# Kernel tuning notes

Hardware: AMD Instinct MI355X
Metric: run time of the kernel (lower is better)

Reference implementation:

```python
import jax, jax.numpy as jnp
import numpy as np

N_NODES = 50000
N_EDGES = 500000
D_IN = 128
HID = 128
OUT = 2
N_REL = 4
BN_EPS = 1e-5


def setup_inputs() -> dict:
    key = jax.random.key(0)
    ks = jax.random.split(key, 14)
    s_in = 1.0 / np.sqrt(D_IN)
    s_h = 1.0 / np.sqrt(HID)
    return {
        "x": jax.random.normal(ks[0], (N_NODES, D_IN), jnp.float32),
        "edge_index": jax.random.randint(ks[1], (N_REL, 2, N_EDGES), 0, N_NODES, jnp.int32),
        "W1": jax.random.normal(ks[2], (N_REL, D_IN, HID), jnp.float32) * s_in,
        "b1": jax.random.normal(ks[3], (N_REL, HID), jnp.float32) * s_in,
        "W2": jax.random.normal(ks[4], (N_REL, HID, HID), jnp.float32) * s_h,
        "b2": jax.random.normal(ks[5], (N_REL, HID), jnp.float32) * s_h,
        "bn_gamma": jnp.ones((HID,), jnp.float32),
        "bn_beta": jnp.zeros((HID,), jnp.float32),
        "lin1_W": jax.random.normal(ks[6], (HID, HID), jnp.float32) * s_h,
        "lin1_b": jax.random.normal(ks[7], (HID,), jnp.float32) * s_h,
        "lin2_W": jax.random.normal(ks[8], (HID, OUT), jnp.float32) * s_h,
        "lin2_b": jax.random.normal(ks[9], (OUT,), jnp.float32) * s_h,
    }


def _gcn(x, ei, W, b):
    # GCNConv: D^-1/2 (A + I) D^-1/2 (X W) + b
    n = x.shape[0]
    h = x @ W                                    # [N, H]
    loops = jnp.arange(n, dtype=ei.dtype)
    src = jnp.concatenate([ei[0], loops])        # add self loops
    dst = jnp.concatenate([ei[1], loops])
    deg = jax.ops.segment_sum(jnp.ones(dst.shape, h.dtype), dst, num_segments=n)
    dinv = jnp.where(deg > 0, jax.lax.rsqrt(deg), 0.0)
    norm = dinv[src] * dinv[dst]                 # [E+N]
    msg = h[src] * norm[:, None]                 # gather + scale
    return jax.ops.segment_sum(msg, dst, num_segments=n) + b


def _hetero(x, edge_index, W, b):
    # HeteroConv with aggr='sum' over the 4 relation types (same src/dst node type)
    out = _gcn(x, edge_index[0], W[0], b[0])
    for r in range(1, N_REL):
        out = out + _gcn(x, edge_index[r], W[r], b[r])
    return out


def reference(x, edge_index, W1, b1, W2, b2, bn_gamma, bn_beta, lin1_W, lin1_b, lin2_W, lin2_b):
    h = jax.nn.relu(_hetero(x, edge_index, W1, b1))
    h = jax.nn.relu(_hetero(h, edge_index, W2, b2))
    # BatchNorm1d (batch statistics, biased variance)
    mean = h.mean(axis=0)
    var = h.var(axis=0)
    h = (h - mean) * jax.lax.rsqrt(var + BN_EPS) * bn_gamma + bn_beta
    h = jax.nn.relu(h @ lin1_W + lin1_b)
    # dropout is identity in eval
    return h @ lin2_W + lin2_b
```

## Files before the change

kernel.cpp:

```cpp
#include <hip/hip_runtime.h>
#include <math.h>

#define NN 50000
#define NE 500000
#define NREL 4
#define D 128
#define RSZ 512
#define NRANGE 98
#define NBK (NREL * NRANGE)
#define BCAP 6144
#define NCH 128
#define CH 3907
#define FCAP 96
#define CAST_BLKS 6250
static constexpr float BN_EPS = 1e-5f;

typedef __attribute__((ext_vector_type(8))) _Float16 half8;
typedef __attribute__((ext_vector_type(4))) float f32x4;

__device__ __forceinline__ unsigned short f2h_bits(float f) {
    _Float16 h = (_Float16)f;
    return __builtin_bit_cast(unsigned short, h);
}

__global__ __launch_bounds__(256) void k_pre(const float* __restrict__ x,
                                             const float* __restrict__ W1, const float* __restrict__ W2,
                                             const float* __restrict__ l1W, const float* __restrict__ b1,
                                             const float* __restrict__ b2,
                                             unsigned short* __restrict__ xb,
                                             unsigned short* __restrict__ Wt1,
                                             unsigned short* __restrict__ Wt2,
                                             unsigned short* __restrict__ Wt3,
                                             float* __restrict__ bs1, float* __restrict__ bs2,
                                             float* __restrict__ bnsum) {
    int blk = blockIdx.x, tid = threadIdx.x;
    if (blk < CAST_BLKS) {
        int i = blk * 256 + tid;
        float4 v = *(const float4*)(x + (size_t)i * 4);
        unsigned short u[4] = {f2h_bits(v.x), f2h_bits(v.y), f2h_bits(v.z), f2h_bits(v.w)};
        *(ushort4*)(xb + (size_t)i * 4) = *(ushort4*)u;
    } else if (blk < CAST_BLKS + 256) {
        int i = (blk - CAST_BLKS) * 256 + tid;
        int kk = i & 511, n = i >> 9;
        Wt1[n * 512 + kk] = f2h_bits(W1[kk * 128 + n]);
        Wt2[n * 512 + kk] = f2h_bits(W2[kk * 128 + n]);
    } else if (blk < CAST_BLKS + 320) {
        int i = (blk - CAST_BLKS - 256) * 256 + tid;
        int kk = i & 127, n = i >> 7;
        Wt3[n * 128 + kk] = f2h_bits(l1W[kk * 128 + n]);
    } else {
        if (tid < 128) {
            bs1[tid] = b1[tid] + b1[128 + tid] + b1[256 + tid] + b1[384 + tid];
            bs2[tid] = b2[tid] + b2[128 + tid] + b2[256 + tid] + b2[384 + tid];
        }
        bnsum[tid] = 0.f;
    }
}

__global__ __launch_bounds__(256) void k_bin(const int* __restrict__ ei,
                                             int* __restrict__ frag,
                                             int* __restrict__ cntg) {
    int c = blockIdx.x, r = blockIdx.y;
    const int* srcp = ei + r * 2 * NE;
    const int* dstp = srcp + NE;
    __shared__ int bins[NRANGE * FCAP];
    __shared__ int cnt[NRANGE];
    int tid = threadIdx.x;
    for (int i = tid; i < NRANGE; i += 256) cnt[i] = 0;
    __syncthreads();
    int e0 = c * CH, e1 = min(e0 + CH, NE);
    for (int e = e0 + tid; e < e1; e += 256) {
        int d = dstp[e];
        int s = srcp[e];
        int q = d >> 9;
        int pos = atomicAdd(&cnt[q], 1);
        if (pos < FCAP) bins[q * FCAP + pos] = s | ((d & 511) << 16);
    }
    __syncthreads();
    int w = tid >> 6, lane = tid & 63;
    for (int q = w; q < NRANGE; q += 4) {
        int k = min(cnt[q], FCAP);
        int gbase = ((r * NRANGE + q) * NCH + c) * FCAP;
        for (int i = lane; i < k; i += 64) frag[gbase + i] = bins[q * FCAP + i];
    }
    for (int q = tid; q < NRANGE; q += 256) cntg[(r * NRANGE + q) * NCH + c] = min(cnt[q], FCAP);
}

__global__ __launch_bounds__(512) void k_sortb(const int* __restrict__ frag,
                                               const int* __restrict__ cntg,
                                               unsigned short* __restrict__ csr,
                                               int* __restrict__ rstart,
                                               int* __restrict__ rend,
                                               float* __restrict__ dinv) {
    int q = blockIdx.x, r = blockIdx.y;
    int blk = r * NRANGE + q;
    int n0 = q * RSZ;
    int nrows = min(RSZ, NN - n0);
    __shared__ int cnts[NCH], cbase[NCH];
    __shared__ int stage[BCAP];
    __shared__ unsigned short csr_s[BCAP];
    __shared__ int hist[RSZ], off[RSZ], cnt2[RSZ];
    int tid = threadIdx.x;
    hist[tid] = 0;
    cnt2[tid] = 0;
    if (tid < NCH) cnts[tid] = cntg[blk * NCH + tid];
    __syncthreads();
    if (tid < NCH) cbase[tid] = cnts[tid];
    __syncthreads();
    for (int d = 1; d < NCH; d <<= 1) {
        int t = 0;
        if (tid < NCH && tid >= d) t = cbase[tid - d];
        __syncthreads();
        if (tid < NCH) cbase[tid] += t;
        __syncthreads();
    }
    if (tid < NCH) cbase[tid] -= cnts[tid];
    __syncthreads();
    int tot = cbase[NCH - 1] + cnts[NCH - 1];
    {
        int g = tid >> 2, l = tid & 3;
        int k = cnts[g], cb = cbase[g];
        int gbase = (blk * NCH + g) * FCAP;
        for (int i = l; i < k; i += 4)
            if (cb + i < BCAP) stage[cb + i] = frag[gbase + i];
    }
    __syncthreads();
    if (tot > BCAP) tot = BCAP;
    for (int i = tid; i < tot; i += 512) atomicAdd(&hist[(stage[i] >> 16) & 511], 1);
    __syncthreads();
    int h = hist[tid];
    if (tid < nrows) dinv[r * NN + n0 + tid] = rsqrtf((float)(h + 1));
    off[tid] = h;
    __syncthreads();
    for (int d = 1; d < RSZ; d <<= 1) {
        int t = (tid >= d) ? off[tid - d] : 0;
        __syncthreads();
        off[tid] += t;
        __syncthreads();
    }
    int excl = off[tid] - h;
    __syncthreads();
    off[tid] = excl;
    int base = blk * BCAP;
    if (tid < nrows) {
        rstart[r * NN + n0 + tid] = base + excl;
        rend[r * NN + n0 + tid] = base + excl + h;
    }
    __syncthreads();
    for (int i = tid; i < tot; i += 512) {
        int v = stage[i];
        int dl = (v >> 16) & 511;
        int p = atomicAdd(&cnt2[dl], 1);
        csr_s[off[dl] + p] = (unsigned short)(v & 0xFFFF);
    }
    __syncthreads();
    for (int i = tid; i < tot; i += 512) csr[base + i] = csr_s[i];
}

__global__ __launch_bounds__(256) void k_wei(const unsigned short* __restrict__ csr,
                                             const float* __restrict__ dinv,
                                             float* __restrict__ wcsr) {
    int gi = blockIdx.x * 256 + threadIdx.x;
    int r = gi / (NRANGE * BCAP);
    int s = csr[gi];
    wcsr[gi] = dinv[r * NN + min(s, NN - 1)];
}

__global__ __launch_bounds__(256) void k_agg(const unsigned short* __restrict__ in,
                                             const unsigned short* __restrict__ csr,
                                             const float* __restrict__ wcsr,
                                             const int* __restrict__ rstart,
                                             const int* __restrict__ rend,
                                             const float* __restrict__ dinv,
                                             unsigned short* __restrict__ Acat) {
    int r = blockIdx.y;
    int wave = threadIdx.x >> 6, lane = threadIdx.x & 63;
    int n = blockIdx.x * 4 + wave;
    if (n >= NN) return;
    int nb = r * NN + n;
    int q = lane >> 4, t = lane & 15;
    const half8* in8 = (const half8*)in;
    half8 us = in8[(size_t)n * 16 + t];
    float wn = dinv[nb];
    int start = rstart[nb], end = rend[nb];
    int deg = end - start;
    float a[8];
#pragma unroll
    for (int j = 0; j < 8; j++) a[j] = 0.f;
    for (int w0 = 0; w0 < deg; w0 += 64) {
        int li = w0 + lane;
        int sv = 0;
        float wv = 0.f;
        if (li < deg) {
            sv = csr[start + li];
            wv = wcsr[start + li];
        }
        int cnt = min(deg - w0, 64);
        for (int b = 0; b < cnt; b += 16) {
            int e = b + q * 4;
            int s0 = __shfl(sv, e + 0), s1 = __shfl(sv, e + 1);
            int s2 = __shfl(sv, e + 2), s3 = __shfl(sv, e + 3);
            float f0 = __shfl(wv, e + 0), f1 = __shfl(wv, e + 1);
            float f2 = __shfl(wv, e + 2), f3 = __shfl(wv, e + 3);
            half8 u0 = in8[s0 * 16 + t];
            half8 u1 = in8[s1 * 16 + t];
            half8 u2 = in8[s2 * 16 + t];
            half8 u3 = in8[s3 * 16 + t];
#pragma unroll
            for (int j = 0; j < 8; j++) a[j] = fmaf((float)u0[j], f0, a[j]);
#pragma unroll
            for (int j = 0; j < 8; j++) a[j] = fmaf((float)u1[j], f1, a[j]);
#pragma unroll
            for (int j = 0; j < 8; j++) a[j] = fmaf((float)u2[j], f2, a[j]);
#pragma unroll
            for (int j = 0; j < 8; j++) a[j] = fmaf((float)u3[j], f3, a[j]);
        }
    }
#pragma unroll
    for (int j = 0; j < 8; j++) {
        a[j] += __shfl_xor(a[j], 16);
        a[j] += __shfl_xor(a[j], 32);
    }
    if (q == 0) {
        _Float16 ob[8];
#pragma unroll
        for (int j = 0; j < 8; j++)
            ob[j] = (_Float16)(wn * fmaf((float)us[j], wn, a[j]));
        *(half8*)(Acat + (size_t)n * 512 + r * 128 + t * 8) = *(half8*)ob;
    }
}

template <int K, bool STATS>
__global__ __launch_bounds__(256) void k_mm(const unsigned short* __restrict__ A,
                                            const unsigned short* __restrict__ Bt,
                                            const float* __restrict__ bias,
                                            unsigned short* __restrict__ C,
                                            float* __restrict__ bnsum) {
    int tid = threadIdx.x;
    int w = tid >> 6, lane = tid & 63;
    int ln = lane & 15, quad = lane >> 4;
    int mwave = blockIdx.x * 256 + w * 64;

    f32x4 acc[4][8];
#pragma unroll
    for (int a = 0; a < 4; a++)
#pragma unroll
        for (int b = 0; b < 8; b++) acc[a][b] = (f32x4){0.f, 0.f, 0.f, 0.f};

    size_t arow[4];
#pragma unroll
    for (int mf = 0; mf < 4; mf++) {
        int m = mwave + mf * 16 + ln;
        arow[mf] = (size_t)min(m, NN - 1) * K;
    }
    size_t brow[8];
#pragma unroll
    for (int nf = 0; nf < 8; nf++) brow[nf] = (size_t)(nf * 16 + ln) * K;

    for (int k0 = 0; k0 < K; k0 += 32) {
        int kof = k0 + quad * 8;
        half8 af[4], bf[8];
#pragma unroll
        for (int mf = 0; mf < 4; mf++) af[mf] = *(const half8*)(A + arow[mf] + kof);
#pragma unroll
        for (int nf = 0; nf < 8; nf++) bf[nf] = *(const half8*)(Bt + brow[nf] + kof);
#pragma unroll
        for (int mf = 0; mf < 4; mf++)
#pragma unroll
            for (int nf = 0; nf < 8; nf++)
                acc[mf][nf] = __builtin_amdgcn_mfma_f32_16x16x32_f16(af[mf], bf[nf], acc[mf][nf], 0, 0, 0);
    }

    float bs[8];
#pragma unroll
    for (int nf = 0; nf < 8; nf++) bs[nf] = bias[nf * 16 + ln];
    float sn[8], qn[8];
#pragma unroll
    for (int nf = 0; nf < 8; nf++) { sn[nf] = 0.f; qn[nf] = 0.f; }

#pragma unroll
    for (int mf = 0; mf < 4; mf++)
#pragma unroll
        for (int nf = 0; nf < 8; nf++)
#pragma unroll
            for (int rg = 0; rg < 4; rg++) {
                int m = mwave + mf * 16 + quad * 4 + rg;
                if (m < NN) {
                    float v = fmaxf(acc[mf][nf][rg] + bs[nf], 0.f);
                    if (STATS) { sn[nf] += v; qn[nf] += v * v; }
                    C[(size_t)m * 128 + nf * 16 + ln] = f2h_bits(v);
                }
            }

    if (STATS) {
#pragma unroll
        for (int nf = 0; nf < 8; nf++) {
            float s = sn[nf], q = qn[nf];
            s += __shfl_xor(s, 16); s += __shfl_xor(s, 32);
            q += __shfl_xor(q, 16); q += __shfl_xor(q, 32);
            if (quad == 0) {
                unsafeAtomicAdd(&bnsum[nf * 16 + ln], s);
                unsafeAtomicAdd(&bnsum[128 + nf * 16 + ln], q);
            }
        }
    }
}

__global__ __launch_bounds__(256) void k_final(const unsigned short* __restrict__ R2,
                                               const float* __restrict__ bnsum,
                                               const float* __restrict__ gamma,
                                               const float* __restrict__ beta,
                                               const unsigned short* __restrict__ Wt3,
                                               const float* __restrict__ l1b,
                                               const float* __restrict__ l2W,
                                               const float* __restrict__ l2b,
                                               float* __restrict__ out) {
    __shared__ float bnp_s[256];
    int tid = threadIdx.x;
    if (tid < 128) {
        float mean = bnsum[tid] / (float)NN;
        float var = bnsum[128 + tid] / (float)NN - mean * mean;
        float sc = gamma[tid] * rsqrtf(var + BN_EPS);
        bnp_s[tid] = sc;
        bnp_s[128 + tid] = beta[tid] - mean * sc;
    }
    __syncthreads();
    int w = tid >> 6, lane = tid & 63;
    int ln = lane & 15, quad = lane >> 4;
    int mwave = blockIdx.x * 256 + w * 64;

    f32x4 acc[4][8];
#pragma unroll
    for (int a = 0; a < 4; a++)
#pragma unroll
        for (int b = 0; b < 8; b++) acc[a][b] = (f32x4){0.f, 0.f, 0.f, 0.f};

    size_t arow[4];
#pragma unroll
    for (int mf = 0; mf < 4; mf++) {
        int m = mwave + mf * 16 + ln;
        arow[mf] = (size_t)min(m, NN - 1) * 128;
    }
    size_t brow[8];
#pragma unroll
    for (int nf = 0; nf < 8; nf++) brow[nf] = (size_t)(nf * 16 + ln) * 128;

    for (int k0 = 0; k0 < 128; k0 += 32) {
        int kof = k0 + quad * 8;
        float scv[8], shv[8];
#pragma unroll
        for (int j = 0; j < 8; j++) {
            scv[j] = bnp_s[kof + j];
            shv[j] = bnp_s[128 + kof + j];
        }
        half8 af[4], bf[8];
#pragma unroll
        for (int mf = 0; mf < 4; mf++) {
            half8 rv = *(const half8*)(R2 + arow[mf] + kof);
            _Float16 ab[8];
#pragma unroll
            for (int j = 0; j < 8; j++)
                ab[j] = (_Float16)(fmaf((float)rv[j], scv[j], shv[j]));
            af[mf] = *(half8*)ab;
        }
#pragma unroll
        for (int nf = 0; nf < 8; nf++) bf[nf] = *(const half8*)(Wt3 + brow[nf] + kof);
#pragma unroll
        for (int mf = 0; mf < 4; mf++)
#pragma unroll
            for (int nf = 0; nf < 8; nf++)
                acc[mf][nf] = __builtin_amdgcn_mfma_f32_16x16x32_f16(af[mf], bf[nf], acc[mf][nf], 0, 0, 0);
    }

    float b1v[8], w0[8], w1[8];
#pragma unroll
    for (int nf = 0; nf < 8; nf++) {
        int n = nf * 16 + ln;
        b1v[nf] = l1b[n];
        w0[nf] = l2W[n * 2];
        w1[nf] = l2W[n * 2 + 1];
    }
    float ob0 = l2b[0], ob1 = l2b[1];
#pragma unroll
    for (int mf = 0; mf < 4; mf++)
#pragma unroll
        for (int rg = 0; rg < 4; rg++) {
            float p0 = 0.f, p1 = 0.f;
#pragma unroll
            for (int nf = 0; nf < 8; nf++) {
                float y = fmaxf(acc[mf][nf][rg] + b1v[nf], 0.f);
                p0 += y * w0[nf];
                p1 += y * w1[nf];
            }
            p0 += __shfl_xor(p0, 1); p0 += __shfl_xor(p0, 2);
            p0 += __shfl_xor(p0, 4); p0 += __shfl_xor(p0, 8);
            p1 += __shfl_xor(p1, 1); p1 += __shfl_xor(p1, 2);
            p1 += __shfl_xor(p1, 4); p1 += __shfl_xor(p1, 8);
            int m = mwave + mf * 16 + quad * 4 + rg;
            if (ln == 0 && m < NN) {
                out[(size_t)m * 2 + 0] = p0 + ob0;
                out[(size_t)m * 2 + 1] = p1 + ob1;
            }
        }
}

extern "C" void kernel_launch(void* const* d_in, const int* in_sizes, int n_in,
                              void* d_out, int out_size, void* d_ws, size_t ws_size,
                              hipStream_t stream) {
    const float* x = (const float*)d_in[0];
    const int* ei = (const int*)d_in[1];
    const float* W1 = (const float*)d_in[2];
    const float* b1 = (const float*)d_in[3];
    const float* W2 = (const float*)d_in[4];
    const float* b2 = (const float*)d_in[5];
    const float* gamma = (const float*)d_in[6];
    const float* beta = (const float*)d_in[7];
    const float* l1W = (const float*)d_in[8];
    const float* l1b = (const float*)d_in[9];
    const float* l2W = (const float*)d_in[10];
    const float* l2b = (const float*)d_in[11];
    float* out = (float*)d_out;

    char* ws = (char*)d_ws;
    size_t off = 0;
    auto alloc = [&](size_t bytes) {
        void* p = ws + off;
        off += (bytes + 255) & ~(size_t)255;
        return p;
    };
    float* dinv = (float*)alloc((size_t)NREL * NN * sizeof(float));
    int* rstart = (int*)alloc((size_t)NREL * NN * sizeof(int));
    int* rend = (int*)alloc((size_t)NREL * NN * sizeof(int));
    unsigned short* csr = (unsigned short*)alloc((size_t)NBK * BCAP * 2);
    unsigned short* xb = (unsigned short*)alloc((size_t)NN * D * 2);
    unsigned short* Acat = (unsigned short*)alloc((size_t)NN * 512 * 2);
    unsigned short* h1b = (unsigned short*)alloc((size_t)NN * D * 2);
    unsigned short* R2b = (unsigned short*)alloc((size_t)NN * D * 2);
    unsigned short* Wt1 = (unsigned short*)alloc(128 * 512 * 2);
    unsigned short* Wt2 = (unsigned short*)alloc(128 * 512 * 2);
    unsigned short* Wt3 = (unsigned short*)alloc(128 * 128 * 2);
    float* bs1 = (float*)alloc(128 * sizeof(float));
    float* bs2 = (float*)alloc(128 * sizeof(float));
    float* bnsum = (float*)alloc(256 * sizeof(float));

    int* frag = (int*)Acat;
    int* cntg = frag + (size_t)NREL * NRANGE * NCH * FCAP;
    float* wcsr = (float*)R2b;

    k_pre<<<CAST_BLKS + 321, 256, 0, stream>>>(x, W1, W2, l1W, b1, b2, xb, Wt1, Wt2, Wt3,
                                               bs1, bs2, bnsum);
    dim3 bgrid(NCH, NREL);
    k_bin<<<bgrid, 256, 0, stream>>>(ei, frag, cntg);
    dim3 sgrid(NRANGE, NREL);
    k_sortb<<<sgrid, 512, 0, stream>>>(frag, cntg, csr, rstart, rend, dinv);
    k_wei<<<(NBK * BCAP) / 256, 256, 0, stream>>>(csr, dinv, wcsr);

    dim3 agrid((NN + 3) / 4, NREL);
    k_agg<<<agrid, 256, 0, stream>>>(xb, csr, wcsr, rstart, rend, dinv, Acat);
    k_mm<512, false><<<(NN + 255) / 256, 256, 0, stream>>>(Acat, Wt1, bs1, h1b, nullptr);
    k_agg<<<agrid, 256, 0, stream>>>(h1b, csr, wcsr, rstart, rend, dinv, Acat);
    k_mm<512, true><<<(NN + 255) / 256, 256, 0, stream>>>(Acat, Wt2, bs2, R2b, bnsum);
    k_final<<<(NN + 255) / 256, 256, 0, stream>>>(R2b, bnsum, gamma, beta, Wt3, l1b, l2W, l2b, out);
}
```

Baseline: 387.0 us.

## Pack CSR index and fp16 weight; aggregate all relations per node in one wave

k_wei now writes a single 32-bit word per edge, holding the 16-bit source index and an fp16 normalization weight, in place of separate index and float-weight arrays. k_agg drops the relation grid dimension: each 16-lane quarter of a wave handles one relation for the same node, and the loop runs to the maximum degree across the four relations. Each step processes 8 or 16 gathers per quarter, and the self-loop term is folded into the accumulator initialization. This removes the cross-quarter reduction, halves the edge metadata loads, and gives more gathers in flight per lane. In exchange, quarters with lower degree sit idle while the wave covers the longest relation, and the edge weight is stored in reduced fp16 precision.

```diff
diff --git a/kernel.cpp b/kernel.cpp
--- a/kernel.cpp
+++ b/kernel.cpp
@@ -21,6 +21,9 @@
 __device__ __forceinline__ unsigned short f2h_bits(float f) {
     _Float16 h = (_Float16)f;
     return __builtin_bit_cast(unsigned short, h);
+}
+__device__ __forceinline__ float hi2f(unsigned p) {
+    return (float)__builtin_bit_cast(_Float16, (unsigned short)(p >> 16));
 }
 
 __global__ __launch_bounds__(256) void k_pre(const float* __restrict__ x,
@@ -159,75 +162,113 @@
 
 __global__ __launch_bounds__(256) void k_wei(const unsigned short* __restrict__ csr,
                                              const float* __restrict__ dinv,
-                                             float* __restrict__ wcsr) {
+                                             unsigned* __restrict__ wpack) {
     int gi = blockIdx.x * 256 + threadIdx.x;
     int r = gi / (NRANGE * BCAP);
     int s = csr[gi];
-    wcsr[gi] = dinv[r * NN + min(s, NN - 1)];
+    float w = dinv[r * NN + min(s, NN - 1)];
+    wpack[gi] = (unsigned)s | ((unsigned)f2h_bits(w) << 16);
 }
 
 __global__ __launch_bounds__(256) void k_agg(const unsigned short* __restrict__ in,
-                                             const unsigned short* __restrict__ csr,
-                                             const float* __restrict__ wcsr,
+                                             const unsigned* __restrict__ wpack,
                                              const int* __restrict__ rstart,
                                              const int* __restrict__ rend,
                                              const float* __restrict__ dinv,
                                              unsigned short* __restrict__ Acat) {
-    int r = blockIdx.y;
     int wave = threadIdx.x >> 6, lane = threadIdx.x & 63;
     int n = blockIdx.x * 4 + wave;
     if (n >= NN) return;
-    int nb = r * NN + n;
-    int q = lane >> 4, t = lane & 15;
+    int t = lane & 15;
+    int base = lane & 48;
+    int nb = (base >> 4) * NN + n;
     const half8* in8 = (const half8*)in;
+    float wn = dinv[nb];
+    int start = rstart[nb];
+    int deg = rend[nb] - start;
+    int dm = deg;
+    dm = max(dm, __shfl_xor(dm, 16));
+    dm = max(dm, __shfl_xor(dm, 32));
     half8 us = in8[(size_t)n * 16 + t];
-    float wn = dinv[nb];
-    int start = rstart[nb], end = rend[nb];
-    int deg = end - start;
     float a[8];
 #pragma unroll
-    for (int j = 0; j < 8; j++) a[j] = 0.f;
-    for (int w0 = 0; w0 < deg; w0 += 64) {
-        int li = w0 + lane;
-        int sv = 0;
-        float wv = 0.f;
-        if (li < deg) {
-            sv = csr[start + li];
-            wv = wcsr[start + li];
-        }
-        int cnt = min(deg - w0, 64);
-        for (int b = 0; b < cnt; b += 16) {
-            int e = b + q * 4;
-            int s0 = __shfl(sv, e + 0), s1 = __shfl(sv, e + 1);
-            int s2 = __shfl(sv, e + 2), s3 = __shfl(sv, e + 3);
-            float f0 = __shfl(wv, e + 0), f1 = __shfl(wv, e + 1);
-            float f2 = __shfl(wv, e + 2), f3 = __shfl(wv, e + 3);
-            half8 u0 = in8[s0 * 16 + t];
-            half8 u1 = in8[s1 * 16 + t];
-            half8 u2 = in8[s2 * 16 + t];
-            half8 u3 = in8[s3 * 16 + t];
-#pragma unroll
-            for (int j = 0; j < 8; j++) a[j] = fmaf((float)u0[j], f0, a[j]);
-#pragma unroll
-            for (int j = 0; j < 8; j++) a[j] = fmaf((float)u1[j], f1, a[j]);
-#pragma unroll
-            for (int j = 0; j < 8; j++) a[j] = fmaf((float)u2[j], f2, a[j]);
-#pragma unroll
-            for (int j = 0; j < 8; j++) a[j] = fmaf((float)u3[j], f3, a[j]);
-        }
-    }
-#pragma unroll
-    for (int j = 0; j < 8; j++) {
-        a[j] += __shfl_xor(a[j], 16);
-        a[j] += __shfl_xor(a[j], 32);
-    }
-    if (q == 0) {
-        _Float16 ob[8];
-#pragma unroll
-        for (int j = 0; j < 8; j++)
-            ob[j] = (_Float16)(wn * fmaf((float)us[j], wn, a[j]));
-        *(half8*)(Acat + (size_t)n * 512 + r * 128 + t * 8) = *(half8*)ob;
-    }
+    for (int j = 0; j < 8; j++) a[j] = wn * (float)us[j];
+
+    for (int w0 = 0; w0 < dm; w0 += 16) {
+        int li = w0 + t;
+        int gi = min(start + li, NBK * BCAP - 1);
+        unsigned pv = wpack[gi];
+        if (li >= deg) pv = 0u;
+        unsigned p0 = __shfl(pv, base + 0), p1 = __shfl(pv, base + 1);
+        unsigned p2 = __shfl(pv, base + 2), p3 = __shfl(pv, base + 3);
+        unsigned p4 = __shfl(pv, base + 4), p5 = __shfl(pv, base + 5);
+        unsigned p6 = __shfl(pv, base + 6), p7 = __shfl(pv, base + 7);
+        {
+            half8 r0 = in8[(p0 & 0xFFFFu) * 16 + t];
+            half8 r1 = in8[(p1 & 0xFFFFu) * 16 + t];
+            half8 r2 = in8[(p2 & 0xFFFFu) * 16 + t];
+            half8 r3 = in8[(p3 & 0xFFFFu) * 16 + t];
+            half8 r4 = in8[(p4 & 0xFFFFu) * 16 + t];
+            half8 r5 = in8[(p5 & 0xFFFFu) * 16 + t];
+            half8 r6 = in8[(p6 & 0xFFFFu) * 16 + t];
+            half8 r7 = in8[(p7 & 0xFFFFu) * 16 + t];
+            float w0f = hi2f(p0), w1f = hi2f(p1), w2f = hi2f(p2), w3f = hi2f(p3);
+            float w4f = hi2f(p4), w5f = hi2f(p5), w6f = hi2f(p6), w7f = hi2f(p7);
+#pragma unroll
+            for (int j = 0; j < 8; j++) a[j] = fmaf((float)r0[j], w0f, a[j]);
+#pragma unroll
+            for (int j = 0; j < 8; j++) a[j] = fmaf((float)r1[j], w1f, a[j]);
+#pragma unroll
+            for (int j = 0; j < 8; j++) a[j] = fmaf((float)r2[j], w2f, a[j]);
+#pragma unroll
+            for (int j = 0; j < 8; j++) a[j] = fmaf((float)r3[j], w3f, a[j]);
+#pragma unroll
+            for (int j = 0; j < 8; j++) a[j] = fmaf((float)r4[j], w4f, a[j]);
+#pragma unroll
+            for (int j = 0; j < 8; j++) a[j] = fmaf((float)r5[j], w5f, a[j]);
+#pragma unroll
+            for (int j = 0; j < 8; j++) a[j] = fmaf((float)r6[j], w6f, a[j]);
+#pragma unroll
+            for (int j = 0; j < 8; j++) a[j] = fmaf((float)r7[j], w7f, a[j]);
+        }
+        if (w0 + 8 >= dm) continue;
+        p0 = __shfl(pv, base + 8);  p1 = __shfl(pv, base + 9);
+        p2 = __shfl(pv, base + 10); p3 = __shfl(pv, base + 11);
+        p4 = __shfl(pv, base + 12); p5 = __shfl(pv, base + 13);
+        p6 = __shfl(pv, base + 14); p7 = __shfl(pv, base + 15);
+        {
+            half8 r0 = in8[(p0 & 0xFFFFu) * 16 + t];
+            half8 r1 = in8[(p1 & 0xFFFFu) * 16 + t];
+            half8 r2 = in8[(p2 & 0xFFFFu) * 16 + t];
+            half8 r3 = in8[(p3 & 0xFFFFu) * 16 + t];
+            half8 r4 = in8[(p4 & 0xFFFFu) * 16 + t];
+            half8 r5 = in8[(p5 & 0xFFFFu) * 16 + t];
+            half8 r6 = in8[(p6 & 0xFFFFu) * 16 + t];
+            half8 r7 = in8[(p7 & 0xFFFFu) * 16 + t];
+            float w0f = hi2f(p0), w1f = hi2f(p1), w2f = hi2f(p2), w3f = hi2f(p3);
+            float w4f = hi2f(p4), w5f = hi2f(p5), w6f = hi2f(p6), w7f = hi2f(p7);
+#pragma unroll
+            for (int j = 0; j < 8; j++) a[j] = fmaf((float)r0[j], w0f, a[j]);
+#pragma unroll
+            for (int j = 0; j < 8; j++) a[j] = fmaf((float)r1[j], w1f, a[j]);
+#pragma unroll
+            for (int j = 0; j < 8; j++) a[j] = fmaf((float)r2[j], w2f, a[j]);
+#pragma unroll
+            for (int j = 0; j < 8; j++) a[j] = fmaf((float)r3[j], w3f, a[j]);
+#pragma unroll
+            for (int j = 0; j < 8; j++) a[j] = fmaf((float)r4[j], w4f, a[j]);
+#pragma unroll
+            for (int j = 0; j < 8; j++) a[j] = fmaf((float)r5[j], w5f, a[j]);
+#pragma unroll
+            for (int j = 0; j < 8; j++) a[j] = fmaf((float)r6[j], w6f, a[j]);
+#pragma unroll
+            for (int j = 0; j < 8; j++) a[j] = fmaf((float)r7[j], w7f, a[j]);
+        }
+    }
+    _Float16 ob[8];
+#pragma unroll
+    for (int j = 0; j < 8; j++) ob[j] = (_Float16)(wn * a[j]);
+    *(half8*)(Acat + (size_t)n * 512 + (base << 3) + t * 8) = *(half8*)ob;
 }
 
 template <int K, bool STATS>
@@ -445,7 +486,7 @@
 
     int* frag = (int*)Acat;
     int* cntg = frag + (size_t)NREL * NRANGE * NCH * FCAP;
-    float* wcsr = (float*)R2b;
+    unsigned* wpack = (unsigned*)R2b;
 
     k_pre<<<CAST_BLKS + 321, 256, 0, stream>>>(x, W1, W2, l1W, b1, b2, xb, Wt1, Wt2, Wt3,
                                                bs1, bs2, bnsum);
@@ -453,12 +494,12 @@
     k_bin<<<bgrid, 256, 0, stream>>>(ei, frag, cntg);
     dim3 sgrid(NRANGE, NREL);
     k_sortb<<<sgrid, 512, 0, stream>>>(frag, cntg, csr, rstart, rend, dinv);
-    k_wei<<<(NBK * BCAP) / 256, 256, 0, stream>>>(csr, dinv, wcsr);
-
-    dim3 agrid((NN + 3) / 4, NREL);
-    k_agg<<<agrid, 256, 0, stream>>>(xb, csr, wcsr, rstart, rend, dinv, Acat);
+    k_wei<<<(NBK * BCAP) / 256, 256, 0, stream>>>(csr, dinv, wpack);
+
+    int agrid = (NN + 3) / 4;
+    k_agg<<<agrid, 256, 0, stream>>>(xb, wpack, rstart, rend, dinv, Acat);
     k_mm<512, false><<<(NN + 255) / 256, 256, 0, stream>>>(Acat, Wt1, bs1, h1b, nullptr);
-    k_agg<<<agrid, 256, 0, stream>>>(h1b, csr, wcsr, rstart, rend, dinv, Acat);
+    k_agg<<<agrid, 256, 0, stream>>>(h1b, wpack, rstart, rend, dinv, Acat);
     k_mm<512, true><<<(NN + 255) / 256, 256, 0, stream>>>(Acat, Wt2, bs2, R2b, bnsum);
     k_final<<<(NN + 255) / 256, 256, 0, stream>>>(R2b, bnsum, gamma, beta, Wt3, l1b, l2W, l2b, out);
 }
```

Result: faster. 367.8 us (-4.9%).
